# Optimization experiments

Measured on AMD Instinct MI355X. Metric: run time of the kernel, lower is better.

The kernel has to match this reference:

```python
import jax, jax.numpy as jnp
import numpy as np

N = 50000   # nodes
E = 400000  # edges
IN_DIM, H1, H2, OUT_DIM = 512, 256, 62, 128


def _param(key, shape, scale=0.05):
    return jax.random.normal(key, shape, dtype=jnp.float32) * scale


def setup_inputs() -> dict:
    key = jax.random.key(0)
    ks = jax.random.split(key, 24)
    x = jax.random.normal(ks[0], (N, IN_DIM), dtype=jnp.float32)
    edge_index_neg = jax.random.randint(ks[1], (2, E), 0, N, dtype=jnp.int64)
    d = {
        "x": x, "edge_index_neg": edge_index_neg,
        # nn.Linear params (W stored as [in, out])
        "W1": _param(ks[2], (IN_DIM, H1)), "b1": _param(ks[3], (H1,)),
        "W2": _param(ks[4], (H1, H2)),    "b2": _param(ks[5], (H2,)),
        "W3": _param(ks[6], (H2, OUT_DIM)), "b3": _param(ks[7], (OUT_DIM,)),
        # GCNConv params: lin weight (no bias) + post-aggregation bias
        "Wg1": _param(ks[8], (H1, H1)),   "bg1": _param(ks[9], (H1,)),
        "Wg2": _param(ks[10], (H2, H2)),  "bg2": _param(ks[11], (H2,)),
        "Wg3": _param(ks[12], (OUT_DIM, OUT_DIM)), "bg3": _param(ks[13], (OUT_DIM,)),
        "Wg4": _param(ks[14], (OUT_DIM, OUT_DIM)), "bg4": _param(ks[15], (OUT_DIM,)),
        "Wg5": _param(ks[16], (OUT_DIM, OUT_DIM)), "bg5": _param(ks[17], (OUT_DIM,)),
        "Wg6": _param(ks[18], (OUT_DIM, OUT_DIM)), "bg6": _param(ks[19], (OUT_DIM,)),
    }
    return d


def _build_norm(edge_index):
    # PyG GCNConv: add self-loops, symmetric normalization D^-1/2 A D^-1/2
    loop = jnp.arange(N, dtype=edge_index.dtype)
    src = jnp.concatenate([edge_index[0], loop])
    dst = jnp.concatenate([edge_index[1], loop])
    deg = jax.ops.segment_sum(jnp.ones_like(dst, dtype=jnp.float32), dst, num_segments=N)
    dinv = jnp.where(deg > 0, jax.lax.rsqrt(jnp.maximum(deg, 1.0)), 0.0)
    norm = dinv[src] * dinv[dst]  # [E+N]
    return src, dst, norm


def _gcn(x, W, b, src, dst, norm):
    h = x @ W                                   # [N, F]
    msg = h[src] * norm[:, None]                # gather + edge scale
    out = jax.ops.segment_sum(msg, dst, num_segments=N)  # scatter-add
    return out + b


def reference(x, edge_index_neg, W1, b1, W2, b2, W3, b3,
              Wg1, bg1, Wg2, bg2, Wg3, bg3, Wg4, bg4, Wg5, bg5, Wg6, bg6):
    src, dst, norm = _build_norm(edge_index_neg)
    relu = jax.nn.relu
    x1l = x @ W1 + b1
    x1 = x1l + relu(_gcn(x1l, Wg1, bg1, src, dst, norm))
    x2l = x1 @ W2 + b2
    x2 = x2l + relu(_gcn(x2l, Wg2, bg2, src, dst, norm))
    x3l = x2 @ W3 + b3
    x3 = x3l + 0.5 * relu(_gcn(x3l, Wg3, bg3, src, dst, norm))
    x4 = x3 + 0.5 * relu(_gcn(x4_in := x3, Wg4, bg4, src, dst, norm))
    x5 = x4 + 0.25 * relu(_gcn(x4, Wg5, bg5, src, dst, norm))
    x6 = x5 + 0.25 * _gcn(x5, Wg6, bg6, src, dst, norm)
    return x6
```

## Files before the change

### kernel.cpp

```cpp
#include <hip/hip_runtime.h>

#define NN 50000
#define NE 400000
#define NBLK 196

using short8 = __attribute__((ext_vector_type(8))) short;
using f32x4  = __attribute__((ext_vector_type(4))) float;
using f32x2  = __attribute__((ext_vector_type(2))) float;
using u16x2  = __attribute__((ext_vector_type(2))) unsigned short;
using u16x4  = __attribute__((ext_vector_type(4))) unsigned short;

__device__ __forceinline__ unsigned short f2b(float f) {
    union { float f; unsigned int u; } x; x.f = f;
    unsigned int u = x.u;
    u += 0x7fffu + ((u >> 16) & 1u);
    return (unsigned short)(u >> 16);
}
__device__ __forceinline__ float b2f(unsigned short u) {
    union { unsigned int u; float f; } x; x.u = ((unsigned int)u) << 16;
    return x.f;
}

#define SWZ(b, row) ((b) ^ (((row) & 7) << 4))

__global__ __launch_bounds__(256) void count_k(const int* __restrict__ dst, int* __restrict__ indeg) {
    int e = blockIdx.x * 256 + threadIdx.x;
    if (e < NE) atomicAdd(&indeg[dst[e]], 1);
}
__global__ __launch_bounds__(256) void scan1_k(const int* __restrict__ indeg, int* __restrict__ tmp,
                                               int* __restrict__ bsum) {
    __shared__ int s[256];
    int t = threadIdx.x, i = blockIdx.x * 256 + t;
    int v = (i < NN) ? indeg[i] : 0;
    s[t] = v; __syncthreads();
    for (int off = 1; off < 256; off <<= 1) {
        int x = (t >= off) ? s[t - off] : 0;
        __syncthreads();
        s[t] += x;
        __syncthreads();
    }
    if (i < NN) tmp[i] = s[t];
    if (t == 255) bsum[blockIdx.x] = s[255];
}
__global__ __launch_bounds__(256) void scan2_k(const int* __restrict__ bsum, int* __restrict__ boff) {
    __shared__ int s[256];
    int t = threadIdx.x;
    int v = (t < NBLK) ? bsum[t] : 0;
    s[t] = v; __syncthreads();
    for (int off = 1; off < 256; off <<= 1) {
        int x = (t >= off) ? s[t - off] : 0;
        __syncthreads();
        s[t] += x;
        __syncthreads();
    }
    if (t < NBLK) boff[t] = s[t] - v;
}
__global__ __launch_bounds__(256) void scan3_k(const int* __restrict__ tmp, const int* __restrict__ indeg,
                                               const int* __restrict__ boff, int* __restrict__ rowptr,
                                               float* __restrict__ dinv) {
    int i = blockIdx.x * 256 + threadIdx.x;
    if (i < NN) {
        rowptr[i] = tmp[i] - indeg[i] + boff[i >> 8];
        dinv[i] = rsqrtf((float)(1 + indeg[i]));
    }
    if (i == 0) rowptr[NN] = NE;
}
__global__ __launch_bounds__(256) void fill_k(const int* __restrict__ src, const int* __restrict__ dst,
                                              const float* __restrict__ dinv, const int* __restrict__ rowptr,
                                              int* __restrict__ cursor, int2* __restrict__ ebn) {
    int e = blockIdx.x * 256 + threadIdx.x;
    if (e >= NE) return;
    int s = src[e], d = dst[e];
    int pos = atomicAdd(&cursor[d], 1);
    ebn[rowptr[d] + pos] = make_int2(s, __float_as_int(dinv[s] * dinv[d]));
}

struct WSegs {
    const float* W[9];
    unsigned short* Wt[9];
    int K[9], N[9], Kp[9];
    int c0[10];
    int* z1; int* z2;
};
__global__ __launch_bounds__(256) void wcast_zero_k(WSegs s) {
    int blk = blockIdx.x;
    if (blk >= s.c0[9]) {
        int i = (blk - s.c0[9]) * 256 + threadIdx.x;
        if (i < NN) { s.z1[i] = 0; s.z2[i] = 0; }
        return;
    }
    #pragma unroll
    for (int g = 0; g < 9; g++) {
        if (blk >= s.c0[g] && blk < s.c0[g + 1]) {
            int idx = (blk - s.c0[g]) * 256 + threadIdx.x;
            int Kp = s.Kp[g];
            int n = idx / Kp, k = idx % Kp;
            float v = (n < s.N[g] && k < s.K[g]) ? s.W[g][(size_t)k * s.N[g] + n] : 0.0f;
            s.Wt[g][idx] = f2b(v);
        }
    }
}

template<bool AF32, int BM, int BN, int NT>
__device__ __forceinline__ void gemm_body(
    const void* __restrict__ Araw, int lda, int Kp,
    const unsigned short* __restrict__ Bt, const float* __restrict__ bias,
    unsigned short* __restrict__ C, int N, int ldc, int M, int r0, char* lds) {
    constexpr int NW = NT / 64;
    constexpr int WC = NW / 2;
    constexpr int WBN = BN / WC;
    constexpr int NF = WBN / 16;
    constexpr int MR = BM / 32;
    constexpr int nA = (BM * 8) / NT;
    constexpr int nB = (BN * 8) / NT;

    int tid = threadIdx.x;
    int lane = tid & 63, wave = tid >> 6;
    int wr = wave / WC, wc = wave % WC;
    int lr = lane & 15, lk = lane >> 4;

    f32x4 acc[MR][NF];
    #pragma unroll
    for (int m = 0; m < MR; m++)
        #pragma unroll
        for (int n = 0; n < NF; n++)
            acc[m][n] = (f32x4){0.f, 0.f, 0.f, 0.f};

    float4 fa0[nA], fa1[nA];
    short8 ra[nA], rb[nB];

    auto LOAD = [&](int k0) {
        #pragma unroll
        for (int c = 0; c < nA; c++) {
            int o = tid + c * NT, row = o >> 3, oct = o & 7;
            int gr = min(r0 + row, M - 1);
            if constexpr (AF32) {
                const float* p = (const float*)Araw + (size_t)gr * lda + k0 + oct * 8;
                fa0[c] = *(const float4*)p;
                fa1[c] = *(const float4*)(p + 4);
            } else {
                ra[c] = *(const short8*)((const unsigned short*)Araw + (size_t)gr * lda + k0 + oct * 8);
            }
        }
        #pragma unroll
        for (int c = 0; c < nB; c++) {
            int o = tid + c * NT, row = o >> 3, oct = o & 7;
            rb[c] = *(const short8*)(Bt + (size_t)row * Kp + k0 + oct * 8);
        }
    };
    auto STORE = [&]() {
        char* AsB = lds;
        char* BsB = lds + BM * 128;
        #pragma unroll
        for (int c = 0; c < nA; c++) {
            int o = tid + c * NT, row = o >> 3, oct = o & 7;
            short8 v;
            if constexpr (AF32) {
                v[0] = (short)f2b(fa0[c].x); v[1] = (short)f2b(fa0[c].y);
                v[2] = (short)f2b(fa0[c].z); v[3] = (short)f2b(fa0[c].w);
                v[4] = (short)f2b(fa1[c].x); v[5] = (short)f2b(fa1[c].y);
                v[6] = (short)f2b(fa1[c].z); v[7] = (short)f2b(fa1[c].w);
            } else {
                v = ra[c];
            }
            *(short8*)(AsB + SWZ(row * 128 + oct * 16, row)) = v;
        }
        #pragma unroll
        for (int c = 0; c < nB; c++) {
            int o = tid + c * NT, row = o >> 3, oct = o & 7;
            *(short8*)(BsB + SWZ(row * 128 + oct * 16, row)) = rb[c];
        }
    };

    int nt = Kp >> 6;
    LOAD(0);
    STORE();
    __syncthreads();
    for (int t = 0; t < nt; t++) {
        if (t + 1 < nt) LOAD((t + 1) << 6);
        char* AsB = lds;
        char* BsB = lds + BM * 128;
        #pragma unroll
        for (int kk = 0; kk < 2; kk++) {
            int kb = kk * 64 + lk * 16;
            short8 a[MR], b[NF];
            #pragma unroll
            for (int m = 0; m < MR; m++) {
                int row = wr * (BM / 2) + m * 16 + lr;
                a[m] = *(short8*)(AsB + SWZ(row * 128 + kb, row));
            }
            #pragma unroll
            for (int n = 0; n < NF; n++) {
                int row = wc * WBN + n * 16 + lr;
                b[n] = *(short8*)(BsB + SWZ(row * 128 + kb, row));
            }
            #pragma unroll
            for (int m = 0; m < MR; m++)
                #pragma unroll
                for (int n = 0; n < NF; n++)
                    acc[m][n] = __builtin_amdgcn_mfma_f32_16x16x32_bf16(a[m], b[n], acc[m][n], 0, 0, 0);
        }
        __syncthreads();
        if (t + 1 < nt) { STORE(); __syncthreads(); }
    }

    constexpr int LDC = BN + 8;
    unsigned short* ldsC = (unsigned short*)lds;
    #pragma unroll
    for (int n = 0; n < NF; n++) {
        int gc = wc * WBN + n * 16 + lr;
        float bv = (bias != nullptr && gc < N) ? bias[gc] : 0.0f;
        bool ok = gc < N;
        #pragma unroll
        for (int m = 0; m < MR; m++)
            #pragma unroll
            for (int j = 0; j < 4; j++) {
                int row = wr * (BM / 2) + m * 16 + lk * 4 + j;
                float v = ok ? acc[m][n][j] + bv : 0.0f;
                ldsC[row * LDC + gc] = f2b(v);
            }
    }
    __syncthreads();
    constexpr int CH = (BM * BN / 8) / NT;
    #pragma unroll
    for (int c = 0; c < CH; c++) {
        int o = tid + c * NT;
        int row = o / (BN / 8), col = (o % (BN / 8)) * 8;
        int gr = r0 + row;
        if (gr < M)
            *(short8*)(C + (size_t)gr * ldc + col) = *(short8*)(ldsC + row * LDC + col);
    }
}

template<int BM, int BN>
constexpr int ldsz() {
    int a = (BM + BN) * 128;
    int b = BM * (BN + 8) * 2;
    return a > b ? a : b;
}

__global__ __launch_bounds__(512) void fused_wide_k(
    const float* __restrict__ x, const unsigned short* __restrict__ W1t, const float* __restrict__ b1,
    unsigned short* __restrict__ C1, const unsigned short* __restrict__ Wg1t,
    unsigned short* __restrict__ C2, int M) {
    __shared__ __align__(16) char lds[ldsz<64, 256>()];
    int r0 = blockIdx.x * 64;
    gemm_body<true, 64, 256, 512>(x, 512, 512, W1t, b1, C1, 256, 256, M, r0, lds);
    __syncthreads();
    gemm_body<false, 64, 256, 512>(C1, 256, 256, Wg1t, nullptr, C2, 256, 256, M, r0, lds);
}

template<int BN>
__global__ __launch_bounds__(256) void fused_pair_k(
    const unsigned short* __restrict__ A1, int lda1, int Kp1,
    const unsigned short* __restrict__ B1t, const float* __restrict__ b1,
    unsigned short* __restrict__ C1, int N,
    const unsigned short* __restrict__ B2t, unsigned short* __restrict__ C2, int M) {
    __shared__ __align__(16) char lds[ldsz<128, BN>()];
    int r0 = blockIdx.x * 128;
    gemm_body<false, 128, BN, 256>(A1, lda1, Kp1, B1t, b1, C1, N, BN, M, r0, lds);
    __syncthreads();
    gemm_body<false, 128, BN, 256>(C1, BN, BN, B2t, nullptr, C2, N, BN, M, r0, lds);
}

__global__ __launch_bounds__(256) void gemm128_k(
    const unsigned short* __restrict__ A, const unsigned short* __restrict__ Bt,
    unsigned short* __restrict__ C, int M) {
    __shared__ __align__(16) char lds[ldsz<128, 128>()];
    gemm_body<false, 128, 128, 256>(A, 128, 128, Bt, nullptr, C, 128, 128, M, blockIdx.x * 128, lds);
}

template<int VEC> struct BV;
template<> struct BV<1> { using T = unsigned short; };
template<> struct BV<2> { using T = u16x2; };
template<> struct BV<4> { using T = u16x4; };
template<int VEC> struct FV;
template<> struct FV<1> { using T = float; };
template<> struct FV<2> { using T = f32x2; };
template<> struct FV<4> { using T = f32x4; };

template<int VEC, int SPLIT, bool OUTF32>
__global__ __launch_bounds__(256) void gather_k(
    const unsigned short* __restrict__ h, const unsigned short* __restrict__ base,
    const float* __restrict__ dinv, const float* __restrict__ bias,
    const int2* __restrict__ ebn, const int* __restrict__ rowptr,
    void* __restrict__ outraw, float alpha, int dorelu, int F) {
    constexpr int ld = 64 * VEC * SPLIT;
    int gw = (blockIdx.x * 256 + threadIdx.x) >> 6;
    int lane = threadIdx.x & 63;
    int w = gw / SPLIT;
    int colbase = (gw % SPLIT) * 64 * VEC;
    if (w >= NN) return;
    using LT = typename BV<VEC>::T;
    const int col = colbase + lane * VEC;

    float acc[VEC];
    float dn = dinv[w];
    {
        LT t = *(const LT*)(h + (size_t)w * ld + col);
        const unsigned short* tu = (const unsigned short*)&t;
        #pragma unroll
        for (int v = 0; v < VEC; v++) acc[v] = b2f(tu[v]) * dn * dn;
    }
    int e = rowptr[w], end = rowptr[w + 1];
    for (; e + 8 <= end; e += 8) {
        long long q[8];
        #pragma unroll
        for (int i = 0; i < 8; i++)
            q[i] = __builtin_nontemporal_load((const long long*)(ebn + e + i));
        LT t[8];
        #pragma unroll
        for (int i = 0; i < 8; i++)
            t[i] = *(const LT*)(h + (size_t)(int)q[i] * ld + col);
        #pragma unroll
        for (int i = 0; i < 8; i++) {
            float nr = __int_as_float((int)(q[i] >> 32));
            const unsigned short* u = (const unsigned short*)&t[i];
            #pragma unroll
            for (int v = 0; v < VEC; v++) acc[v] += b2f(u[v]) * nr;
        }
    }
    for (; e + 2 <= end; e += 2) {
        long long q0 = __builtin_nontemporal_load((const long long*)(ebn + e));
        long long q1 = __builtin_nontemporal_load((const long long*)(ebn + e + 1));
        LT t0 = *(const LT*)(h + (size_t)(int)q0 * ld + col);
        LT t1 = *(const LT*)(h + (size_t)(int)q1 * ld + col);
        float n0 = __int_as_float((int)(q0 >> 32)), n1 = __int_as_float((int)(q1 >> 32));
        const unsigned short* u0 = (const unsigned short*)&t0;
        const unsigned short* u1 = (const unsigned short*)&t1;
        #pragma unroll
        for (int v = 0; v < VEC; v++) acc[v] += b2f(u0[v]) * n0 + b2f(u1[v]) * n1;
    }
    if (e < end) {
        long long q0 = __builtin_nontemporal_load((const long long*)(ebn + e));
        LT t0 = *(const LT*)(h + (size_t)(int)q0 * ld + col);
        float n0 = __int_as_float((int)(q0 >> 32));
        const unsigned short* u0 = (const unsigned short*)&t0;
        #pragma unroll
        for (int v = 0; v < VEC; v++) acc[v] += b2f(u0[v]) * n0;
    }
    LT bt = *(const LT*)(base + (size_t)w * ld + col);
    const unsigned short* bu = (const unsigned short*)&bt;
    if (OUTF32) {
        typename FV<VEC>::T ot;
        float* of = (float*)&ot;
        #pragma unroll
        for (int v = 0; v < VEC; v++) {
            int f = col + v;
            float a = acc[v] + ((f < F) ? bias[f] : 0.0f);
            if (dorelu) a = fmaxf(a, 0.0f);
            of[v] = (f < F) ? b2f(bu[v]) + alpha * a : 0.0f;
        }
        *(typename FV<VEC>::T*)((float*)outraw + (size_t)w * ld + col) = ot;
    } else {
        LT ot;
        unsigned short* ou = (unsigned short*)&ot;
        #pragma unroll
        for (int v = 0; v < VEC; v++) {
            int f = col + v;
            float a = acc[v] + ((f < F) ? bias[f] : 0.0f);
            if (dorelu) a = fmaxf(a, 0.0f);
            float res = (f < F) ? b2f(bu[v]) + alpha * a : 0.0f;
            ou[v] = f2b(res);
        }
        *(LT*)((unsigned short*)outraw + (size_t)w * ld + col) = ot;
    }
}

extern "C" void kernel_launch(void* const* d_in, const int* in_sizes, int n_in,
                              void* d_out, int out_size, void* d_ws, size_t ws_size,
                              hipStream_t stream) {
    const float* x   = (const float*)d_in[0];
    const int*   ei  = (const int*)d_in[1];
    const float* W1  = (const float*)d_in[2];  const float* b1  = (const float*)d_in[3];
    const float* W2  = (const float*)d_in[4];  const float* b2  = (const float*)d_in[5];
    const float* W3  = (const float*)d_in[6];  const float* b3  = (const float*)d_in[7];
    const float* Wg1 = (const float*)d_in[8];  const float* bg1 = (const float*)d_in[9];
    const float* Wg2 = (const float*)d_in[10]; const float* bg2 = (const float*)d_in[11];
    const float* Wg3 = (const float*)d_in[12]; const float* bg3 = (const float*)d_in[13];
    const float* Wg4 = (const float*)d_in[14]; const float* bg4 = (const float*)d_in[15];
    const float* Wg5 = (const float*)d_in[16]; const float* bg5 = (const float*)d_in[17];
    const float* Wg6 = (const float*)d_in[18]; const float* bg6 = (const float*)d_in[19];
    const int* srcv = ei;
    const int* dstv = ei + NE;

    float* dinv = (float*)d_ws;
    unsigned short* hA = (unsigned short*)(dinv + 51200);
    unsigned short* hB = hA + (size_t)NN * 256;
    unsigned short* hC = hB + (size_t)NN * 256;
    unsigned short* W1t  = hC + (size_t)NN * 256;
    unsigned short* Wg1t = W1t  + 256 * 512;
    unsigned short* W2t  = Wg1t + 256 * 256;
    unsigned short* Wg2t = W2t  + 64 * 256;
    unsigned short* W3t  = Wg2t + 64 * 64;
    unsigned short* Wg3t = W3t  + 128 * 64;
    unsigned short* Wg4t = Wg3t + 128 * 128;
    unsigned short* Wg5t = Wg4t + 128 * 128;
    unsigned short* Wg6t = Wg5t + 128 * 128;
    int* indeg  = (int*)(Wg6t + 128 * 128);
    int* cursor = indeg + 51200;
    int* tmp    = cursor + 51200;
    int* rowptr = tmp + 51200;
    int* bsum   = rowptr + 51264;
    int* boff   = bsum + 256;
    int2* ebn   = (int2*)(boff + 256);

    {
        WSegs s;
        const float* Ws[9] = {W1, Wg1, W2, Wg2, W3, Wg3, Wg4, Wg5, Wg6};
        unsigned short* Wts[9] = {W1t, Wg1t, W2t, Wg2t, W3t, Wg3t, Wg4t, Wg5t, Wg6t};
        int Ks[9]  = {512, 256, 256, 62, 62, 128, 128, 128, 128};
        int Ns[9]  = {256, 256, 62, 62, 128, 128, 128, 128, 128};
        int Kps[9] = {512, 256, 256, 64, 64, 128, 128, 128, 128};
        int Nps[9] = {256, 256, 64, 64, 128, 128, 128, 128, 128};
        int c = 0;
        for (int g = 0; g < 9; g++) {
            s.W[g] = Ws[g]; s.Wt[g] = Wts[g];
            s.K[g] = Ks[g]; s.N[g] = Ns[g]; s.Kp[g] = Kps[g];
            s.c0[g] = c;
            c += (Kps[g] * Nps[g]) / 256;
        }
        s.c0[9] = c;
        s.z1 = indeg; s.z2 = cursor;
        wcast_zero_k<<<c + NBLK, 256, 0, stream>>>(s);
    }
    count_k<<<(NE + 255) / 256, 256, 0, stream>>>(dstv, indeg);
    scan1_k<<<NBLK, 256, 0, stream>>>(indeg, tmp, bsum);
    scan2_k<<<1, 256, 0, stream>>>(bsum, boff);
    scan3_k<<<NBLK, 256, 0, stream>>>(tmp, indeg, boff, rowptr, dinv);
    fill_k<<<(NE + 255) / 256, 256, 0, stream>>>(srcv, dstv, dinv, rowptr, cursor, ebn);

    const int GX1 = (NN + 63) / 64;
    const int GX2 = (NN + 127) / 128;
    const int GG1 = (NN * 64 + 255) / 256;

    fused_wide_k<<<GX1, 512, 0, stream>>>(x, W1t, b1, hA, Wg1t, hB, NN);
    gather_k<4, 1, false><<<GG1, 256, 0, stream>>>(hB, hA, dinv, bg1, ebn, rowptr, hC, 1.0f, 1, 256);
    fused_pair_k<64><<<GX2, 256, 0, stream>>>(hC, 256, 256, W2t, b2, hA, 62, Wg2t, hB, NN);
    gather_k<1, 1, false><<<GG1, 256, 0, stream>>>(hB, hA, dinv, bg2, ebn, rowptr, hC, 1.0f, 1, 62);
    fused_pair_k<128><<<GX2, 256, 0, stream>>>(hC, 64, 64, W3t, b3, hA, 128, Wg3t, hB, NN);
    gather_k<2, 1, false><<<GG1, 256, 0, stream>>>(hB, hA, dinv, bg3, ebn, rowptr, hC, 0.5f, 1, 128);
    gemm128_k<<<GX2, 256, 0, stream>>>(hC, Wg4t, hA, NN);
    gather_k<2, 1, false><<<GG1, 256, 0, stream>>>(hA, hC, dinv, bg4, ebn, rowptr, hB, 0.5f, 1, 128);
    gemm128_k<<<GX2, 256, 0, stream>>>(hB, Wg5t, hA, NN);
    gather_k<2, 1, false><<<GG1, 256, 0, stream>>>(hA, hB, dinv, bg5, ebn, rowptr, hC, 0.25f, 1, 128);
    gemm128_k<<<GX2, 256, 0, stream>>>(hC, Wg6t, hA, NN);
    gather_k<2, 1, true><<<GG1, 256, 0, stream>>>(hA, hC, dinv, bg6, ebn, rowptr, d_out, 0.25f, 0, 128);
}
```

Baseline: 359.8 us.

## Keep stage-1 GEMM output in LDS as swizzled A operand for fused second GEMM

The first GEMM of each fused pair now writes its bf16 tile straight into a swizzled LDS region laid out as the A operand of the second GEMM. The second GEMM reads A from LDS and streams only B from global memory, so it no longer re-reads C1 from global. gemm128_k is also specialised with a hand-unrolled K loop. The larger LDS footprint (for example 72KB for the wide kernel) may lower occupancy.

```diff
diff --git a/kernel.cpp b/kernel.cpp
--- a/kernel.cpp
+++ b/kernel.cpp
@@ -102,10 +102,11 @@
 }
 
 template<bool AF32, int BM, int BN, int NT>
-__device__ __forceinline__ void gemm_body(
+__device__ __forceinline__ void gemm_stage1(
     const void* __restrict__ Araw, int lda, int Kp,
     const unsigned short* __restrict__ Bt, const float* __restrict__ bias,
-    unsigned short* __restrict__ C, int N, int ldc, int M, int r0, char* lds) {
+    unsigned short* __restrict__ C, int N, int ldc, int M, int r0,
+    char* lds, char* aswz) {
     constexpr int NW = NT / 64;
     constexpr int WC = NW / 2;
     constexpr int WBN = BN / WC;
@@ -204,20 +205,20 @@
         if (t + 1 < nt) { STORE(); __syncthreads(); }
     }
 
-    constexpr int LDC = BN + 8;
-    unsigned short* ldsC = (unsigned short*)lds;
     #pragma unroll
     for (int n = 0; n < NF; n++) {
         int gc = wc * WBN + n * 16 + lr;
         float bv = (bias != nullptr && gc < N) ? bias[gc] : 0.0f;
         bool ok = gc < N;
+        int sub = gc >> 6, kin = gc & 63;
+        char* base = aswz + sub * (BM * 128) + (kin & 7) * 2;
         #pragma unroll
         for (int m = 0; m < MR; m++)
             #pragma unroll
             for (int j = 0; j < 4; j++) {
                 int row = wr * (BM / 2) + m * 16 + lk * 4 + j;
                 float v = ok ? acc[m][n][j] + bv : 0.0f;
-                ldsC[row * LDC + gc] = f2b(v);
+                *(unsigned short*)(base + SWZ(row * 128 + (kin >> 3) * 16, row)) = f2b(v);
             }
     }
     __syncthreads();
@@ -225,29 +226,122 @@
     #pragma unroll
     for (int c = 0; c < CH; c++) {
         int o = tid + c * NT;
-        int row = o / (BN / 8), col = (o % (BN / 8)) * 8;
+        int row = o / (BN / 8), cg = o % (BN / 8);
+        int sub = cg >> 3, oct = cg & 7;
+        short8 v = *(short8*)(aswz + sub * (BM * 128) + SWZ(row * 128 + oct * 16, row));
+        int gr = r0 + row;
+        if (gr < M)
+            *(short8*)(C + (size_t)gr * ldc + sub * 64 + oct * 8) = v;
+    }
+}
+
+template<int BM, int ON, int NT>
+__device__ __forceinline__ void gemm_stage2(
+    const char* __restrict__ aswz, const unsigned short* __restrict__ Bt, int Kp,
+    unsigned short* __restrict__ C, int N, int ldc, int M, int r0,
+    char* ldsB, unsigned short* ldsC) {
+    constexpr int NW = NT / 64;
+    constexpr int WC = NW / 2;
+    constexpr int WBN = ON / WC;
+    constexpr int NF = WBN / 16;
+    constexpr int MR = BM / 32;
+    constexpr int nB = (ON * 8) / NT;
+
+    int tid = threadIdx.x;
+    int lane = tid & 63, wave = tid >> 6;
+    int wr = wave / WC, wc = wave % WC;
+    int lr = lane & 15, lk = lane >> 4;
+
+    f32x4 acc[MR][NF];
+    #pragma unroll
+    for (int m = 0; m < MR; m++)
+        #pragma unroll
+        for (int n = 0; n < NF; n++)
+            acc[m][n] = (f32x4){0.f, 0.f, 0.f, 0.f};
+
+    short8 rb[nB];
+    auto LOADB = [&](int k0) {
+        #pragma unroll
+        for (int c = 0; c < nB; c++) {
+            int o = tid + c * NT, row = o >> 3, oct = o & 7;
+            rb[c] = *(const short8*)(Bt + (size_t)row * Kp + k0 + oct * 8);
+        }
+    };
+    auto STOREB = [&]() {
+        #pragma unroll
+        for (int c = 0; c < nB; c++) {
+            int o = tid + c * NT, row = o >> 3, oct = o & 7;
+            *(short8*)(ldsB + SWZ(row * 128 + oct * 16, row)) = rb[c];
+        }
+    };
+
+    int nt = Kp >> 6;
+    LOADB(0);
+    STOREB();
+    __syncthreads();
+    for (int t = 0; t < nt; t++) {
+        if (t + 1 < nt) LOADB((t + 1) << 6);
+        const char* AsB = aswz + t * (BM * 128);
+        #pragma unroll
+        for (int kk = 0; kk < 2; kk++) {
+            int kb = kk * 64 + lk * 16;
+            short8 a[MR], b[NF];
+            #pragma unroll
+            for (int m = 0; m < MR; m++) {
+                int row = wr * (BM / 2) + m * 16 + lr;
+                a[m] = *(short8*)(AsB + SWZ(row * 128 + kb, row));
+            }
+            #pragma unroll
+            for (int n = 0; n < NF; n++) {
+                int row = wc * WBN + n * 16 + lr;
+                b[n] = *(short8*)(ldsB + SWZ(row * 128 + kb, row));
+            }
+            #pragma unroll
+            for (int m = 0; m < MR; m++)
+                #pragma unroll
+                for (int n = 0; n < NF; n++)
+                    acc[m][n] = __builtin_amdgcn_mfma_f32_16x16x32_bf16(a[m], b[n], acc[m][n], 0, 0, 0);
+        }
+        __syncthreads();
+        if (t + 1 < nt) { STOREB(); __syncthreads(); }
+    }
+
+    constexpr int LDC = ON + 8;
+    #pragma unroll
+    for (int n = 0; n < NF; n++) {
+        int gc = wc * WBN + n * 16 + lr;
+        bool ok = gc < N;
+        #pragma unroll
+        for (int m = 0; m < MR; m++)
+            #pragma unroll
+            for (int j = 0; j < 4; j++) {
+                int row = wr * (BM / 2) + m * 16 + lk * 4 + j;
+                float v = ok ? acc[m][n][j] : 0.0f;
+                ldsC[row * LDC + gc] = f2b(v);
+            }
+    }
+    __syncthreads();
+    constexpr int CH = (BM * ON / 8) / NT;
+    #pragma unroll
+    for (int c = 0; c < CH; c++) {
+        int o = tid + c * NT;
+        int row = o / (ON / 8), col = (o % (ON / 8)) * 8;
         int gr = r0 + row;
         if (gr < M)
             *(short8*)(C + (size_t)gr * ldc + col) = *(short8*)(ldsC + row * LDC + col);
     }
-}
-
-template<int BM, int BN>
-constexpr int ldsz() {
-    int a = (BM + BN) * 128;
-    int b = BM * (BN + 8) * 2;
-    return a > b ? a : b;
 }
 
 __global__ __launch_bounds__(512) void fused_wide_k(
     const float* __restrict__ x, const unsigned short* __restrict__ W1t, const float* __restrict__ b1,
     unsigned short* __restrict__ C1, const unsigned short* __restrict__ Wg1t,
     unsigned short* __restrict__ C2, int M) {
-    __shared__ __align__(16) char lds[ldsz<64, 256>()];
+    __shared__ __align__(16) char lds[73728];
+    char* aswz = lds + 40960;
     int r0 = blockIdx.x * 64;
-    gemm_body<true, 64, 256, 512>(x, 512, 512, W1t, b1, C1, 256, 256, M, r0, lds);
-    __syncthreads();
-    gemm_body<false, 64, 256, 512>(C1, 256, 256, Wg1t, nullptr, C2, 256, 256, M, r0, lds);
+    gemm_stage1<true, 64, 256, 512>(x, 512, 512, W1t, b1, C1, 256, 256, M, r0, lds, aswz);
+    __syncthreads();
+    gemm_stage2<64, 256, 512>(aswz, Wg1t, 256, C2, 256, 256, M, r0, lds, (unsigned short*)lds);
 }
 
 template<int BN>
@@ -256,18 +350,116 @@
     const unsigned short* __restrict__ B1t, const float* __restrict__ b1,
     unsigned short* __restrict__ C1, int N,
     const unsigned short* __restrict__ B2t, unsigned short* __restrict__ C2, int M) {
-    __shared__ __align__(16) char lds[ldsz<128, BN>()];
+    constexpr int LOOP1 = (128 + BN) * 128;
+    constexpr int ASWZ  = 128 * BN * 2;
+    constexpr int LDSC  = 128 * (BN + 8) * 2;
+    constexpr int TOT   = LOOP1 + ASWZ > LDSC ? LOOP1 + ASWZ : LDSC;
+    __shared__ __align__(16) char lds[TOT];
+    char* aswz = lds + LOOP1;
     int r0 = blockIdx.x * 128;
-    gemm_body<false, 128, BN, 256>(A1, lda1, Kp1, B1t, b1, C1, N, BN, M, r0, lds);
-    __syncthreads();
-    gemm_body<false, 128, BN, 256>(C1, BN, BN, B2t, nullptr, C2, N, BN, M, r0, lds);
+    gemm_stage1<false, 128, BN, 256>(A1, lda1, Kp1, B1t, b1, C1, N, BN, M, r0, lds, aswz);
+    __syncthreads();
+    gemm_stage2<128, BN, 256>(aswz, B2t, BN, C2, N, BN, M, r0, lds, (unsigned short*)lds);
 }
 
 __global__ __launch_bounds__(256) void gemm128_k(
     const unsigned short* __restrict__ A, const unsigned short* __restrict__ Bt,
     unsigned short* __restrict__ C, int M) {
-    __shared__ __align__(16) char lds[ldsz<128, 128>()];
-    gemm_body<false, 128, 128, 256>(A, 128, 128, Bt, nullptr, C, 128, 128, M, blockIdx.x * 128, lds);
+    constexpr int BM = 128, BN = 128, NT = 256;
+    constexpr int TOT = 128 * (128 + 8) * 2;
+    __shared__ __align__(16) char lds[TOT];
+    constexpr int NF = 4, MR = 4;
+    int tid = threadIdx.x;
+    int lane = tid & 63, wave = tid >> 6;
+    int wr = wave >> 1, wc = wave & 1;
+    int lr = lane & 15, lk = lane >> 4;
+    int r0 = blockIdx.x * BM;
+
+    f32x4 acc[MR][NF];
+    #pragma unroll
+    for (int m = 0; m < MR; m++)
+        #pragma unroll
+        for (int n = 0; n < NF; n++)
+            acc[m][n] = (f32x4){0.f, 0.f, 0.f, 0.f};
+
+    short8 ra[4], rb[4];
+    auto LOAD = [&](int k0) {
+        #pragma unroll
+        for (int c = 0; c < 4; c++) {
+            int o = tid + c * NT, row = o >> 3, oct = o & 7;
+            int gr = min(r0 + row, M - 1);
+            ra[c] = *(const short8*)(A + (size_t)gr * 128 + k0 + oct * 8);
+        }
+        #pragma unroll
+        for (int c = 0; c < 4; c++) {
+            int o = tid + c * NT, row = o >> 3, oct = o & 7;
+            rb[c] = *(const short8*)(Bt + (size_t)row * 128 + k0 + oct * 8);
+        }
+    };
+    auto STORE = [&]() {
+        #pragma unroll
+        for (int c = 0; c < 4; c++) {
+            int o = tid + c * NT, row = o >> 3, oct = o & 7;
+            *(short8*)(lds + SWZ(row * 128 + oct * 16, row)) = ra[c];
+        }
+        #pragma unroll
+        for (int c = 0; c < 4; c++) {
+            int o = tid + c * NT, row = o >> 3, oct = o & 7;
+            *(short8*)(lds + BM * 128 + SWZ(row * 128 + oct * 16, row)) = rb[c];
+        }
+    };
+
+    LOAD(0);
+    STORE();
+    __syncthreads();
+    for (int t = 0; t < 2; t++) {
+        if (t == 0) LOAD(64);
+        #pragma unroll
+        for (int kk = 0; kk < 2; kk++) {
+            int kb = kk * 64 + lk * 16;
+            short8 a[MR], b[NF];
+            #pragma unroll
+            for (int m = 0; m < MR; m++) {
+                int row = wr * 64 + m * 16 + lr;
+                a[m] = *(short8*)(lds + SWZ(row * 128 + kb, row));
+            }
+            #pragma unroll
+            for (int n = 0; n < NF; n++) {
+                int row = wc * 64 + n * 16 + lr;
+                b[n] = *(short8*)(lds + BM * 128 + SWZ(row * 128 + kb, row));
+            }
+            #pragma unroll
+            for (int m = 0; m < MR; m++)
+                #pragma unroll
+                for (int n = 0; n < NF; n++)
+                    acc[m][n] = __builtin_amdgcn_mfma_f32_16x16x32_bf16(a[m], b[n], acc[m][n], 0, 0, 0);
+        }
+        __syncthreads();
+        if (t == 0) { STORE(); __syncthreads(); }
+    }
+
+    constexpr int LDC = BN + 8;
+    unsigned short* ldsC = (unsigned short*)lds;
+    #pragma unroll
+    for (int n = 0; n < NF; n++) {
+        int gc = wc * 64 + n * 16 + lr;
+        #pragma unroll
+        for (int m = 0; m < MR; m++)
+            #pragma unroll
+            for (int j = 0; j < 4; j++) {
+                int row = wr * 64 + m * 16 + lk * 4 + j;
+                ldsC[row * LDC + gc] = f2b(acc[m][n][j]);
+            }
+    }
+    __syncthreads();
+    #pragma unroll
+    for (int c = 0; c < 8; c++) {
+        int o = tid + c * NT;
+        int row = o >> 4, col = (o & 15) * 8;
+        int gr = r0 + row;
+        if (gr < M)
+            *(short8*)(C + (size_t)gr * 128 + col) = *(short8*)(ldsC + row * LDC + col);
+    }
 }
 
 template<int VEC> struct BV;
```

Result: no change. 355.5 us (-1.2%).
